# Kernel optimization log

Hardware: AMD Instinct MI355X
Metric: run time of the kernel (lower is better)

Reference implementation:

```python
import jax, jax.numpy as jnp
import numpy as np

B, N, S = 8, 8192, 1024
K = 16          # max_degree
HIDDEN = 192    # hidden_dim, divisible by 2*ndim -> no padding in sincos embed
NDIM = 3
MAX_WAVELENGTH = 10000.0


def sincos_embed(coords, dim, ndim):
    # Continuous sin/cos embedding: dim//ndim channels per coordinate,
    # half sin / half cos, geometric frequencies (UPT-style).
    dpw = dim // ndim                          # dims per coordinate (even)
    ar = jnp.arange(0, dpw, 2, dtype=coords.dtype)
    omega = 1.0 / (MAX_WAVELENGTH ** (ar / dpw))   # (dpw/2,)
    out = coords[..., None] * omega            # (..., ndim, dpw/2)
    emb = jnp.concatenate([jnp.sin(out), jnp.cos(out)], axis=-1)  # (..., ndim, dpw)
    return emb.reshape(*coords.shape[:-1], dim)


def knn_gather(x, sidx, k):
    # x: (B,N,ndim), sidx: (B,S) -> (B,S,k,ndim) coords of k nearest neighbors.
    # Equivalent to the original dense NxN dists[sidx] + argsort[:, :k],
    # but only computes the S rows that are used and uses top_k.
    def per_sample(sx, si):
        sp = sx[si]                                            # (S, ndim)
        d = jnp.sum((sp[:, None, :] - sx[None, :, :]) ** 2, -1)  # (S, N)
        _, nbr = jax.lax.top_k(-d, k)                          # k smallest dists
        return sx[nbr]                                         # (S, k, ndim)
    return jax.vmap(per_sample)(x, sidx)


def setup_inputs() -> dict:
    key = jax.random.key(0)
    ks = jax.random.split(key, 6)
    scale = 0.02
    return {
        "input_points": jax.random.normal(ks[0], (B, N, NDIM), dtype=jnp.float32),
        "supernode_idxs": jax.random.randint(ks[1], (B, S), 0, N),
        "w_in": jax.random.normal(ks[2], (NDIM, HIDDEN), dtype=jnp.float32) * scale,
        "b_in": jnp.zeros((HIDDEN,), dtype=jnp.float32),
        "w1": jax.random.normal(ks[3], (HIDDEN, HIDDEN), dtype=jnp.float32) * scale,
        "b1": jnp.zeros((HIDDEN,), dtype=jnp.float32),
        "w2": jax.random.normal(ks[4], (HIDDEN, HIDDEN), dtype=jnp.float32) * scale,
        "b2": jnp.zeros((HIDDEN,), dtype=jnp.float32),
    }


def reference(input_points, supernode_idxs, w_in, b_in, w1, b1, w2, b2):
    nbr = knn_gather(input_points, supernode_idxs, K)      # (B,S,K,3)
    # input projection + continuous sincos positional embedding
    h = nbr @ w_in + b_in + sincos_embed(nbr, HIDDEN, NDIM)  # (B,S,K,H)
    # message net: Dense -> gelu -> Dense
    h = jax.nn.gelu(h @ w1 + b1)
    h = h @ w2 + b2
    # mean-pool over neighbors per supernode
    return jnp.mean(h, axis=-2)                            # (B,S,H)
```

## Files before the change

### kernel.cpp

```cpp
#include <hip/hip_runtime.h>
#include <stdint.h>

#define NB   8
#define NPTS 8192
#define NS   1024
#define NK   16
#define NH   192
#define KP1  224
#define HROW 196
#define QTR  2048

typedef float    f32x4 __attribute__((ext_vector_type(4)));
typedef short    s16x8 __attribute__((ext_vector_type(8)));
typedef uint32_t u32;
typedef unsigned long long u64;

constexpr float OMEGA[32] = {
  1.0f, 0.74989420933245585f, 0.56234132519034907f, 0.42169650342858223f,
  0.31622776601683794f, 0.23713737056616552f, 0.17782794100389229f, 0.13335214321633237f,
  0.1f, 0.074989420933245585f, 0.056234132519034907f, 0.042169650342858223f,
  0.031622776601683794f, 0.023713737056616552f, 0.017782794100389229f, 0.013335214321633237f,
  0.01f, 0.0074989420933245585f, 0.0056234132519034907f, 0.0042169650342858223f,
  0.0031622776601683794f, 0.0023713737056616552f, 0.0017782794100389229f, 0.0013335214321633237f,
  0.001f, 0.00074989420933245585f, 0.00056234132519034907f, 0.00042169650342858223f,
  0.00031622776601683794f, 0.00023713737056616552f, 0.00017782794100389229f, 0.00013335214321633237f };

__device__ __forceinline__ uint16_t f2bf(float f) {
  u32 u = __float_as_uint(f);
  return (uint16_t)((u + 0x7FFFu + ((u >> 16) & 1u)) >> 16);
}
__device__ __forceinline__ u32 pk2bf(float f0, float f1) {
  return ((__float_as_uint(f0) + 0x8000u) >> 16) |
         ((__float_as_uint(f1) + 0x8000u) & 0xFFFF0000u);
}
__device__ __forceinline__ float rflf(float v) {
  return __uint_as_float(__builtin_amdgcn_readfirstlane(__float_as_uint(v)));
}
__device__ __forceinline__ u64 rfl64(u64 v) {
  u32 lo = __builtin_amdgcn_readfirstlane((u32)v);
  u32 hi = __builtin_amdgcn_readfirstlane((u32)(v >> 32));
  return ((u64)hi << 32) | lo;
}

__global__ void __launch_bounds__(64) prep_weights(
    const float* __restrict__ w_in, const float* __restrict__ b_in,
    const float* __restrict__ w1, const float* __restrict__ b1,
    const float* __restrict__ w2,
    uint16_t* __restrict__ wT1e, uint16_t* __restrict__ wT2) {
  const int n = blockIdx.x, t = threadIdx.x;
  float p0 = 0, p1 = 0, p2 = 0, pb = 0;
  #pragma unroll
  for (int kk = 0; kk < 3; ++kk) {
    int c = kk * 64 + t;
    float w1cn = w1[c * NH + n];
    wT1e[n * KP1 + c] = f2bf(w1cn);
    wT2 [n * NH  + c] = f2bf(w2[c * NH + n]);
    p0 = fmaf(w_in[0 * NH + c], w1cn, p0);
    p1 = fmaf(w_in[1 * NH + c], w1cn, p1);
    p2 = fmaf(w_in[2 * NH + c], w1cn, p2);
    pb = fmaf(b_in[c], w1cn, pb);
  }
  #pragma unroll
  for (int off = 32; off; off >>= 1) {
    p0 += __shfl_down(p0, off);
    p1 += __shfl_down(p1, off);
    p2 += __shfl_down(p2, off);
    pb += __shfl_down(pb, off);
  }
  if (t == 0) {
    wT1e[n * KP1 + 192] = f2bf(p0);
    wT1e[n * KP1 + 193] = f2bf(p1);
    wT1e[n * KP1 + 194] = f2bf(p2);
    wT1e[n * KP1 + 195] = f2bf(pb + b1[n]);
  }
  if (t >= 4 && t < 32) wT1e[n * KP1 + 192 + t] = 0;
}

__global__ void __launch_bounds__(512, 8) knn_kernel(const float* __restrict__ pts,
                                                     const int* __restrict__ sidx,
                                                     u64* __restrict__ keys) {
  __shared__ float4 P4[QTR];
  const int bid = blockIdx.x;
  const int b = bid >> 7;
  const int chunk = (bid >> 2) & 31;
  const int quarter = bid & 3;
  const int pbase = quarter * QTR;
  const float* pb = pts + ((size_t)b * NPTS + pbase) * 3;
  for (int i = threadIdx.x; i < QTR; i += 512)
    P4[i] = float4{pb[3 * i], pb[3 * i + 1], pb[3 * i + 2], 0.0f};
  __syncthreads();
  const int wave = threadIdx.x >> 6, lane = threadIdx.x & 63;
  const int sbase = chunk * 32 + wave * 4;

  float sx[4], sy[4], sz[4], minD[4], Td[4];
  u32 minT[4];
  u64 arr[4], T[4];
  #pragma unroll
  for (int q = 0; q < 4; ++q) {
    int si = __builtin_amdgcn_readfirstlane(sidx[b * NS + sbase + q]);
    const float* qp = pts + ((size_t)b * NPTS + si) * 3;
    sx[q] = rflf(qp[0]); sy[q] = rflf(qp[1]); sz[q] = rflf(qp[2]);
    minD[q] = __uint_as_float(0x7F800000u);
    minT[q] = 0xFFFFFFFFu;
  }

  for (int t = 0; t < QTR / 64; ++t) {
    float4 p = P4[t * 64 + lane];
    #pragma unroll
    for (int q = 0; q < 4; ++q) {
      float dx = p.x - sx[q], dy = p.y - sy[q], dz = p.z - sz[q];
      float d = __fadd_rn(__fadd_rn(__fmul_rn(dx, dx), __fmul_rn(dy, dy)),
                          __fmul_rn(dz, dz));
      bool c = d < minD[q];
      minD[q] = c ? d : minD[q];
      minT[q] = c ? (u32)t : minT[q];
    }
  }

  #pragma unroll
  for (int q = 0; q < 4; ++q) {
    u32 gidx = (u32)(pbase + (int)minT[q] * 64 + lane);
    u64 key = ((u64)__float_as_uint(minD[q]) << 32) | gidx;
    #pragma unroll
    for (int k = 2; k <= 64; k <<= 1) {
      #pragma unroll
      for (int jj = k >> 1; jj > 0; jj >>= 1) {
        u64 p = __shfl_xor(key, jj);
        bool takeMin = (((lane & jj) == 0) == ((lane & k) == 0));
        key = (takeMin == (p < key)) ? p : key;
      }
    }
    arr[q] = (lane < 16) ? key : ~0ull;
    T[q] = rfl64(__shfl(key, 15));
    Td[q] = __uint_as_float((u32)(T[q] >> 32));
  }

  for (int t = 0; t < QTR / 64; ++t) {
    float4 p = P4[t * 64 + lane];
    #pragma unroll
    for (int q = 0; q < 4; ++q) {
      float dx = p.x - sx[q], dy = p.y - sy[q], dz = p.z - sz[q];
      float d = __fadd_rn(__fadd_rn(__fmul_rn(dx, dx), __fmul_rn(dy, dy)),
                          __fmul_rn(dz, dz));
      u64 ball = __ballot(d <= Td[q] && minT[q] != (u32)t);
      if (ball) {
        u64 key = ((u64)__float_as_uint(d) << 32) | (u32)(pbase + t * 64 + lane);
        do {
          int src = __builtin_ctzll(ball);
          ball &= ball - 1;
          u64 k2 = rfl64(__shfl(key, src));
          if (k2 < T[q]) {
            int r = __popcll(__ballot(arr[q] < k2));
            u64 up = __shfl_up(arr[q], 1);
            if (lane == r) arr[q] = k2;
            else if (lane > r && lane < 16) arr[q] = up;
            T[q] = rfl64(__shfl(arr[q], 15));
            Td[q] = __uint_as_float((u32)(T[q] >> 32));
          }
        } while (ball);
      }
    }
  }
  #pragma unroll
  for (int q = 0; q < 4; ++q)
    if (lane < 16)
      keys[((size_t)(b * NS + sbase + q)) * 64 + quarter * 16 + lane] = arr[q];
}

__device__ __forceinline__ float h0ch(int c, float c0, float c1, float c2) {
  int dd = c >> 6, i = c & 63, m = i & 31;
  float coord = (dd == 0) ? c0 : ((dd == 1) ? c1 : c2);
  float arg = coord * OMEGA[m];
  return (i < 32) ? __sinf(arg) : __cosf(arg);
}

__device__ __forceinline__ float gelu_f(float x) {
  float v = -1.5957691216057308f * __fmaf_rn(0.044715f * x, x * x, x);
  return x * __builtin_amdgcn_rcpf(1.0f + __expf(v));
}

__global__ void __launch_bounds__(256, 3) mlp_kernel(
    const float* __restrict__ pts, const u64* __restrict__ keys,
    const float* __restrict__ b2v,
    const uint16_t* __restrict__ wT1e, const uint16_t* __restrict__ wT2,
    float* __restrict__ out) {
  __shared__ uint16_t hbuf[128 * HROW];
  __shared__ float crdL[128][3];
  __shared__ int nbrL[128];
  const int g = blockIdx.x, tid = threadIdx.x;
  const int wave = tid >> 6, lane = tid & 63;
  const int lrow = lane & 15, lg = lane >> 4;
  const int ns = wave;

  #pragma unroll
  for (int ii = 0; ii < 2; ++ii) {
    int q = ii * 4 + wave;
    int list = lane >> 4, pos = lane & 15;
    int rpos = (list & 1) ? (15 - pos) : pos;
    u64 key = keys[((size_t)g * 8 + q) * 64 + list * 16 + rpos];
    #pragma unroll
    for (int jj = 16; jj > 0; jj >>= 1) {
      u64 p = __shfl_xor(key, jj);
      bool takeMin = (((lane & jj) == 0) == ((lane & 32) == 0));
      key = (takeMin == (p < key)) ? p : key;
    }
    #pragma unroll
    for (int jj = 32; jj > 0; jj >>= 1) {
      u64 p = __shfl_xor(key, jj);
      bool takeMin = ((lane & jj) == 0);
      key = (takeMin == (p < key)) ? p : key;
    }
    if (lane < 16) nbrL[q * 16 + lane] = (int)(u32)key;
  }
  __syncthreads();

  {
    int r = tid >> 1, half = tid & 1;
    int grow = g * 128 + r;
    int b = grow >> 14;
    int pidx = nbrL[r];
    const float* pp = pts + ((size_t)b * NPTS + pidx) * 3;
    float c0 = pp[0], c1 = pp[1], c2 = pp[2];
    uint16_t* hrow = hbuf + r * HROW;
    if (half == 0) {
      crdL[r][0] = c0; crdL[r][1] = c1; crdL[r][2] = c2;
      #pragma unroll
      for (int jj = 0; jj < 24; ++jj) {
        const int c = jj * 4;
        uint2 pk;
        pk.x = pk2bf(h0ch(c,     c0, c1, c2), h0ch(c + 1, c0, c1, c2));
        pk.y = pk2bf(h0ch(c + 2, c0, c1, c2), h0ch(c + 3, c0, c1, c2));
        *(uint2*)(hrow + c) = pk;
      }
    } else {
      #pragma unroll
      for (int jj = 0; jj < 24; ++jj) {
        const int c = 96 + jj * 4;
        uint2 pk;
        pk.x = pk2bf(h0ch(c,     c0, c1, c2), h0ch(c + 1, c0, c1, c2));
        pk.y = pk2bf(h0ch(c + 2, c0, c1, c2), h0ch(c + 3, c0, c1, c2));
        *(uint2*)(hrow + c) = pk;
      }
    }
  }
  __syncthreads();

  f32x4 acc1[3][8] = {};
  {
    const uint16_t* wbase = wT1e + (size_t)(ns * 48 + lrow) * KP1 + lg * 8;
    uint4 anx[2][3];
    #pragma unroll
    for (int nt = 0; nt < 3; ++nt) {
      anx[0][nt] = *(const uint4*)(wbase + nt * 16 * KP1);
      anx[1][nt] = *(const uint4*)(wbase + nt * 16 * KP1 + 32);
    }
    #pragma unroll
    for (int kk = 0; kk < 7; ++kk) {
      uint4 acur[3];
      #pragma unroll
      for (int nt = 0; nt < 3; ++nt) acur[nt] = anx[kk & 1][nt];
      if (kk < 5) {
        #pragma unroll
        for (int nt = 0; nt < 3; ++nt)
          anx[kk & 1][nt] = *(const uint4*)(wbase + nt * 16 * KP1 + (kk + 2) * 32);
      }
      s16x8 bm[8];
      if (kk < 6) {
        #pragma unroll
        for (int mt = 0; mt < 8; ++mt)
          bm[mt] = __builtin_bit_cast(s16x8,
                     *(const uint4*)(hbuf + (mt * 16 + lrow) * HROW + kk * 32 + lg * 8));
      } else {
        #pragma unroll
        for (int mt = 0; mt < 8; ++mt) {
          uint4 t{0, 0, 0, 0};
          if (lg == 0) {
            const float* cp = crdL[mt * 16 + lrow];
            t.x = pk2bf(cp[0], cp[1]);
            t.y = pk2bf(cp[2], 1.0f);
          }
          bm[mt] = __builtin_bit_cast(s16x8, t);
        }
      }
      #pragma unroll
      for (int nt = 0; nt < 3; ++nt)
        #pragma unroll
        for (int mt = 0; mt < 8; ++mt)
          acc1[nt][mt] = __builtin_amdgcn_mfma_f32_16x16x32_bf16(
              __builtin_bit_cast(s16x8, acur[nt]), bm[mt], acc1[nt][mt], 0, 0, 0);
    }
  }
  __syncthreads();

  {
    #pragma unroll
    for (int nt = 0; nt < 3; ++nt) {
      #pragma unroll
      for (int mt = 0; mt < 8; ++mt) {
        uint2 pk;
        pk.x = pk2bf(gelu_f(acc1[nt][mt][0]), gelu_f(acc1[nt][mt][1]));
        pk.y = pk2bf(gelu_f(acc1[nt][mt][2]), gelu_f(acc1[nt][mt][3]));
        *(uint2*)(hbuf + (mt * 16 + lrow) * HROW + ns * 48 + nt * 16 + lg * 4) = pk;
      }
    }
  }
  __syncthreads();

  f32x4 acc2[8][3] = {};
  {
    const uint16_t* w2base = wT2 + (size_t)(ns * 48 + lrow) * NH + lg * 8;
    uint4 bnx[2][3];
    #pragma unroll
    for (int nt = 0; nt < 3; ++nt) {
      bnx[0][nt] = *(const uint4*)(w2base + nt * 16 * NH);
      bnx[1][nt] = *(const uint4*)(w2base + nt * 16 * NH + 32);
    }
    #pragma unroll
    for (int kk = 0; kk < 6; ++kk) {
      uint4 bcur[3];
      #pragma unroll
      for (int nt = 0; nt < 3; ++nt) bcur[nt] = bnx[kk & 1][nt];
      if (kk < 4) {
        #pragma unroll
        for (int nt = 0; nt < 3; ++nt)
          bnx[kk & 1][nt] = *(const uint4*)(w2base + nt * 16 * NH + (kk + 2) * 32);
      }
      s16x8 am[8];
      #pragma unroll
      for (int mt = 0; mt < 8; ++mt)
        am[mt] = __builtin_bit_cast(s16x8,
                   *(const uint4*)(hbuf + (mt * 16 + lrow) * HROW + kk * 32 + lg * 8));
      #pragma unroll
      for (int mt = 0; mt < 8; ++mt)
        #pragma unroll
        for (int nt = 0; nt < 3; ++nt)
          acc2[mt][nt] = __builtin_amdgcn_mfma_f32_16x16x32_bf16(
              am[mt], __builtin_bit_cast(s16x8, bcur[nt]), acc2[mt][nt], 0, 0, 0);
    }
  }

  {
    #pragma unroll
    for (int mt = 0; mt < 8; ++mt) {
      #pragma unroll
      for (int nt = 0; nt < 3; ++nt) {
        float ssum = acc2[mt][nt][0] + acc2[mt][nt][1] + acc2[mt][nt][2] + acc2[mt][nt][3];
        ssum += __shfl_xor(ssum, 16);
        ssum += __shfl_xor(ssum, 32);
        if (lane < 16) {
          int col = ns * 48 + nt * 16 + lrow;
          out[(size_t)(g * 8 + mt) * NH + col] = ssum * 0.0625f + b2v[col];
        }
      }
    }
  }
}

extern "C" void kernel_launch(void* const* d_in, const int* in_sizes, int n_in,
                              void* d_out, int out_size, void* d_ws, size_t ws_size,
                              hipStream_t stream) {
  (void)in_sizes; (void)n_in; (void)out_size; (void)ws_size;
  const float* pts  = (const float*)d_in[0];
  const int*   sidx = (const int*)d_in[1];
  const float* w_in = (const float*)d_in[2];
  const float* b_in = (const float*)d_in[3];
  const float* w1   = (const float*)d_in[4];
  const float* b1   = (const float*)d_in[5];
  const float* w2   = (const float*)d_in[6];
  const float* b2   = (const float*)d_in[7];
  float* out = (float*)d_out;

  u64* keys = (u64*)d_ws;
  uint16_t* wT1e = (uint16_t*)((char*)d_ws + (size_t)NB * NS * 64 * 8);
  uint16_t* wT2  = wT1e + NH * KP1;

  hipLaunchKernelGGL(prep_weights, dim3(NH), dim3(64), 0, stream,
                     w_in, b_in, w1, b1, w2, wT1e, wT2);

  hipLaunchKernelGGL(knn_kernel, dim3(NB * 128), dim3(512), 0, stream,
                     pts, sidx, keys);

  hipLaunchKernelGGL(mlp_kernel, dim3(NB * NS / 8), dim3(256), 0, stream,
                     pts, keys, b2, wT1e, wT2, out);
}
```

Before: 92.61 us.

## Track top-2 per lane in KNN scan and replace second full pass with targeted rescans

Each lane now keeps its two smallest distances (with their tile indices) during the single scan over the point quarter, instead of only the minimum. After the wave sort, the second-smallest candidates are merged, and only the lanes whose second-best still beats the current 16th-best threshold get their column of 32 points rescanned. This replaces the second full pass over all 2048 points per query with a small amount of selective work. In exchange the first pass does a few more ALU ops and uses more registers, and lanes where many true neighbours cluster can trigger serialized rescans.

```diff
diff --git a/kernel.cpp b/kernel.cpp
--- a/kernel.cpp
+++ b/kernel.cpp
@@ -92,16 +92,18 @@
   const int wave = threadIdx.x >> 6, lane = threadIdx.x & 63;
   const int sbase = chunk * 32 + wave * 4;
 
-  float sx[4], sy[4], sz[4], minD[4], Td[4];
-  u32 minT[4];
+  float sx[4], sy[4], sz[4], Td[4];
+  float m1D[4], m2D[4];
+  u32 m1T[4], m2T[4];
   u64 arr[4], T[4];
   #pragma unroll
   for (int q = 0; q < 4; ++q) {
     int si = __builtin_amdgcn_readfirstlane(sidx[b * NS + sbase + q]);
     const float* qp = pts + ((size_t)b * NPTS + si) * 3;
     sx[q] = rflf(qp[0]); sy[q] = rflf(qp[1]); sz[q] = rflf(qp[2]);
-    minD[q] = __uint_as_float(0x7F800000u);
-    minT[q] = 0xFFFFFFFFu;
+    m1D[q] = __uint_as_float(0x7F800000u);
+    m2D[q] = __uint_as_float(0x7F800000u);
+    m1T[q] = 0xFFFFFFFFu; m2T[q] = 0xFFFFFFFFu;
   }
 
   for (int t = 0; t < QTR / 64; ++t) {
@@ -111,16 +113,19 @@
       float dx = p.x - sx[q], dy = p.y - sy[q], dz = p.z - sz[q];
       float d = __fadd_rn(__fadd_rn(__fmul_rn(dx, dx), __fmul_rn(dy, dy)),
                           __fmul_rn(dz, dz));
-      bool c = d < minD[q];
-      minD[q] = c ? d : minD[q];
-      minT[q] = c ? (u32)t : minT[q];
+      bool c1 = d < m1D[q];
+      bool c2 = d < m2D[q];
+      m2D[q] = fminf(fmaxf(d, m1D[q]), m2D[q]);
+      m2T[q] = c2 ? (c1 ? m1T[q] : (u32)t) : m2T[q];
+      m1D[q] = fminf(d, m1D[q]);
+      m1T[q] = c1 ? (u32)t : m1T[q];
     }
   }
 
   #pragma unroll
   for (int q = 0; q < 4; ++q) {
-    u32 gidx = (u32)(pbase + (int)minT[q] * 64 + lane);
-    u64 key = ((u64)__float_as_uint(minD[q]) << 32) | gidx;
+    u64 key = ((u64)__float_as_uint(m1D[q]) << 32)
+            | (u32)(pbase + (int)m1T[q] * 64 + lane);
     #pragma unroll
     for (int k = 2; k <= 64; k <<= 1) {
       #pragma unroll
@@ -133,31 +138,51 @@
     arr[q] = (lane < 16) ? key : ~0ull;
     T[q] = rfl64(__shfl(key, 15));
     Td[q] = __uint_as_float((u32)(T[q] >> 32));
-  }
-
-  for (int t = 0; t < QTR / 64; ++t) {
-    float4 p = P4[t * 64 + lane];
-    #pragma unroll
-    for (int q = 0; q < 4; ++q) {
-      float dx = p.x - sx[q], dy = p.y - sy[q], dz = p.z - sz[q];
-      float d = __fadd_rn(__fadd_rn(__fmul_rn(dx, dx), __fmul_rn(dy, dy)),
-                          __fmul_rn(dz, dz));
-      u64 ball = __ballot(d <= Td[q] && minT[q] != (u32)t);
-      if (ball) {
-        u64 key = ((u64)__float_as_uint(d) << 32) | (u32)(pbase + t * 64 + lane);
-        do {
-          int src = __builtin_ctzll(ball);
-          ball &= ball - 1;
-          u64 k2 = rfl64(__shfl(key, src));
-          if (k2 < T[q]) {
-            int r = __popcll(__ballot(arr[q] < k2));
-            u64 up = __shfl_up(arr[q], 1);
-            if (lane == r) arr[q] = k2;
-            else if (lane > r && lane < 16) arr[q] = up;
-            T[q] = rfl64(__shfl(arr[q], 15));
-            Td[q] = __uint_as_float((u32)(T[q] >> 32));
-          }
-        } while (ball);
+    (void)Td;
+
+    u64 key2 = ((u64)__float_as_uint(m2D[q]) << 32)
+             | (u32)(pbase + (int)m2T[q] * 64 + lane);
+    u64 ball = __ballot(key2 < T[q]);
+    while (ball) {
+      int src = __builtin_ctzll(ball);
+      ball &= ball - 1;
+      u64 k2 = rfl64(__shfl(key2, src));
+      if (k2 < T[q]) {
+        int r = __popcll(__ballot(arr[q] < k2));
+        u64 up = __shfl_up(arr[q], 1);
+        if (lane == r) arr[q] = k2;
+        else if (lane > r && lane < 16) arr[q] = up;
+        T[q] = rfl64(__shfl(arr[q], 15));
+      }
+    }
+
+    u64 flags = __ballot(key2 < T[q]);
+    while (flags) {
+      int j = __builtin_ctzll(flags);
+      flags &= flags - 1;
+      u32 ex1 = __builtin_amdgcn_readfirstlane(__shfl(m1T[q], j));
+      u32 ex2 = __builtin_amdgcn_readfirstlane(__shfl(m2T[q], j));
+      u64 ckey = ~0ull;
+      if (lane < QTR / 64) {
+        float4 p = P4[lane * 64 + j];
+        float dx = p.x - sx[q], dy = p.y - sy[q], dz = p.z - sz[q];
+        float d = __fadd_rn(__fadd_rn(__fmul_rn(dx, dx), __fmul_rn(dy, dy)),
+                            __fmul_rn(dz, dz));
+        ckey = ((u64)__float_as_uint(d) << 32) | (u32)(pbase + lane * 64 + j);
+        if ((u32)lane == ex1 || (u32)lane == ex2) ckey = ~0ull;
+      }
+      u64 b2 = __ballot(ckey < T[q]);
+      while (b2) {
+        int src = __builtin_ctzll(b2);
+        b2 &= b2 - 1;
+        u64 k2 = rfl64(__shfl(ckey, src));
+        if (k2 < T[q]) {
+          int r = __popcll(__ballot(arr[q] < k2));
+          u64 up = __shfl_up(arr[q], 1);
+          if (lane == r) arr[q] = k2;
+          else if (lane > r && lane < 16) arr[q] = up;
+          T[q] = rfl64(__shfl(arr[q], 15));
+        }
       }
     }
   }
```

Result: no change. 92.21 us (-0.4%).
